# Optimization experiments

Hardware: AMD Instinct MI355X
Metric: run time of the kernel (lower is better)

Reference implementation:

```python
import jax, jax.numpy as jnp
import numpy as np

# CMSBlockLinear block-ELL sparse linear forward.
# values: [R, K, B, B] active weight tiles (out_tile x in_tile)
# col_indices: [R, K] int32, which input block-column each tile multiplies
# y[b,s, r*B+i] = sum_k sum_j values[r,k,i,j] * x[b,s, col_indices[r,k]*B + j] + bias

IN_FEATURES = 2048
OUT_FEATURES = 2048
TILE = 16
DENSITY = 0.25
R = OUT_FEATURES // TILE   # 128
C = IN_FEATURES // TILE    # 128
K = max(1, int(C * DENSITY))  # 32
BATCH, SEQ = 4, 512


def setup_inputs() -> dict:
    key = jax.random.key(0)
    kx, kv, kc = jax.random.split(key, 3)
    x = jax.random.normal(kx, (BATCH, SEQ, IN_FEATURES), dtype=jnp.float32)
    # Kaiming-normal init as in _reset_parameters: std = gain('relu') / sqrt(K*B)
    std = np.sqrt(2.0) / np.sqrt(K * TILE)
    values = jax.random.normal(kv, (R, K, TILE, TILE), dtype=jnp.float32) * std
    # K distinct column indices per row (random topology, as in _initialize_topology)
    rng = np.random.default_rng(0)
    col_np = np.stack([rng.permutation(C)[:K] for _ in range(R)]).astype(np.int32)
    col_indices = jnp.asarray(col_np)
    bias = jnp.zeros((OUT_FEATURES,), dtype=jnp.float32)
    return {"x": x, "values": values, "col_indices": col_indices, "bias": bias}


def reference(x, values, col_indices, bias):
    bs, sl, _ = x.shape
    Rr, Kk, B, _ = values.shape
    Cc = x.shape[-1] // B
    x_blocks = x.reshape(bs, sl, Cc, B)                 # [b, s, C, B]
    # Gather the K active input blocks for every output row: [b, s, R, K, B]
    x_gathered = x_blocks[:, :, col_indices, :]
    # Batched small-block matmul and reduce over K tiles: [b, s, R, B]
    out = jnp.einsum("bsrkj,rkij->bsri", x_gathered, values)
    return out.reshape(bs, sl, Rr * B) + bias
```

## Files before the change

### kernel.cpp

```cpp
#include <hip/hip_runtime.h>
#include <hip/hip_bf16.h>

#define TOKS 2048
#define FEAT 2048
#define NR   128
#define KB   32
#define RB   32
#define TT   32

typedef __attribute__((ext_vector_type(8))) short bf16x8;
typedef __attribute__((ext_vector_type(4))) float f32x4;

__device__ __forceinline__ unsigned short f2bf(float f) {
    unsigned u = __builtin_bit_cast(unsigned, f);
    u += 0x7FFFu + ((u >> 16) & 1u);
    return (unsigned short)(u >> 16);
}

__device__ __forceinline__ bf16x8 pack8(float4 a, float4 b) {
    bf16x8 r;
    r[0] = (short)f2bf(a.x); r[1] = (short)f2bf(a.y);
    r[2] = (short)f2bf(a.z); r[3] = (short)f2bf(a.w);
    r[4] = (short)f2bf(b.x); r[5] = (short)f2bf(b.y);
    r[6] = (short)f2bf(b.z); r[7] = (short)f2bf(b.w);
    return r;
}

__global__ __launch_bounds__(256) void cvt_values_kernel(const float* __restrict__ v,
                                                         unsigned short* __restrict__ o,
                                                         int n) {
    int i = (blockIdx.x * 256 + threadIdx.x) * 4;
    if (i + 3 < n) {
        float4 f = *reinterpret_cast<const float4*>(v + i);
        ushort4 r;
        r.x = f2bf(f.x); r.y = f2bf(f.y); r.z = f2bf(f.z); r.w = f2bf(f.w);
        *reinterpret_cast<ushort4*>(o + i) = r;
    }
}

template<bool VB16>
__global__ __launch_bounds__(512) void bsp_kernel(const float* __restrict__ x,
                                                  const void* __restrict__ values,
                                                  const int* __restrict__ cols,
                                                  const float* __restrict__ bias,
                                                  float* __restrict__ out) {
    __shared__ __align__(16) unsigned short xs[TT * FEAT];

    int bid  = blockIdx.x;
    int xcd  = bid & 7, slot = bid >> 3;
    int tg   = xcd * 8 + (slot >> 2);
    int rg   = slot & 3;
    int tok0 = tg * TT;
    int r0   = rg * RB;
    int tid  = threadIdx.x;

    {
        int tr = tid >> 8;
        int ch = tid & 255;
        #pragma unroll 4
        for (int it = 0; it < TT / 2; ++it) {
            int t = it * 2 + tr;
            const float4* p = reinterpret_cast<const float4*>(
                x + (size_t)(tok0 + t) * FEAT + ch * 8);
            float4 a = p[0], b = p[1];
            int off = (t << 12) + ((ch << 4) ^ ((t & 7) << 4));
            *reinterpret_cast<bf16x8*>(reinterpret_cast<char*>(xs) + off) = pack8(a, b);
        }
    }
    __syncthreads();

    int wave = tid >> 6;
    int lane = tid & 63;
    int n = lane & 15;
    int g = lane >> 4;
    int h = g & 1;
    int q = g >> 1;

    int mrow = n << 12;
    int axor = (n & 7) << 4;

    #pragma unroll 1
    for (int rr = 0; rr < 4; ++rr) {
        int r = r0 + wave * 4 + rr;
        int cbase = __builtin_amdgcn_readfirstlane(r) * KB;

        bf16x8 bfrag[16];
        int aaddr[16];
        if (VB16) {
            const unsigned short* vbl = reinterpret_cast<const unsigned short*>(values)
                + ((size_t)r << 13) + (q << 8) + (n << 4) + (h << 3);
            #pragma unroll
            for (int t = 0; t < 16; ++t) {
                bfrag[t] = *reinterpret_cast<const bf16x8*>(vbl + t * 512);
                int c0 = cols[cbase + 2 * t];
                int c1 = cols[cbase + 2 * t + 1];
                int c  = q ? c1 : c0;
                aaddr[t] = mrow + (((c << 5) + (h << 4)) ^ axor);
            }
        } else {
            const float* vfl = reinterpret_cast<const float*>(values)
                + ((size_t)r << 13) + (q << 8) + (n << 4) + (h << 3);
            #pragma unroll
            for (int t = 0; t < 16; ++t) {
                const float4* pv = reinterpret_cast<const float4*>(vfl + t * 512);
                bfrag[t] = pack8(pv[0], pv[1]);
                int c0 = cols[cbase + 2 * t];
                int c1 = cols[cbase + 2 * t + 1];
                int c  = q ? c1 : c0;
                aaddr[t] = mrow + (((c << 5) + (h << 4)) ^ axor);
            }
        }

        float fb = bias[(r << 4) + n];

        #pragma unroll
        for (int sx = 0; sx < 2; ++sx) {
            f32x4 acc = {0.f, 0.f, 0.f, 0.f};
            const char* xb = reinterpret_cast<const char*>(xs) + (sx << 16);
            #pragma unroll
            for (int t = 0; t < 16; ++t) {
                bf16x8 af = *reinterpret_cast<const bf16x8*>(xb + aaddr[t]);
                acc = __builtin_amdgcn_mfma_f32_16x16x32_bf16(af, bfrag[t], acc, 0, 0, 0);
            }
            int trow = tok0 + (sx << 4) + (g << 2);
            size_t ob = (size_t)trow * 2048 + (r << 4) + n;
            #pragma unroll
            for (int p = 0; p < 4; ++p)
                out[ob + (size_t)p * 2048] = acc[p] + fb;
        }
    }
}

extern "C" void kernel_launch(void* const* d_in, const int* in_sizes, int n_in,
                              void* d_out, int out_size, void* d_ws, size_t ws_size,
                              hipStream_t stream) {
    const float* x      = (const float*)d_in[0];
    const float* values = (const float*)d_in[1];
    const int*   cols   = (const int*)d_in[2];
    const float* bias   = (const float*)d_in[3];
    float*       out    = (float*)d_out;

    const int nv = NR * KB * 16 * 16;
    const int grid = (TOKS / TT) * (NR / RB);

    if (ws_size >= (size_t)nv * sizeof(unsigned short)) {
        unsigned short* vb = (unsigned short*)d_ws;
        cvt_values_kernel<<<nv / (256 * 4), 256, 0, stream>>>(values, vb, nv);
        bsp_kernel<true><<<grid, 512, 0, stream>>>(x, vb, cols, bias, out);
    } else {
        bsp_kernel<false><<<grid, 512, 0, stream>>>(x, values, cols, bias, out);
    }
}
```

Measured before the change: 22.76 us.

## Use 1024-thread blocks, prefetch weight fragments before barrier, split MFMA accumulators

Doubles the block to 16 waves so each wave handles 2 output rows instead of 4, and splits the x staging loop across 4 token rows per iteration. The first row's weight fragments and column addresses are loaded before the LDS barrier, overlapping global loads with the x staging. The MFMA chain is split into two independent accumulators to shorten the dependency chain. The cost is higher register pressure under launch_bounds(1024,4), with a risk of spills.

```diff
diff --git a/kernel.cpp b/kernel.cpp
--- a/kernel.cpp
+++ b/kernel.cpp
@@ -39,11 +39,40 @@
 }
 
 template<bool VB16>
-__global__ __launch_bounds__(512) void bsp_kernel(const float* __restrict__ x,
-                                                  const void* __restrict__ values,
-                                                  const int* __restrict__ cols,
-                                                  const float* __restrict__ bias,
-                                                  float* __restrict__ out) {
+__device__ __forceinline__ void load_frags(const void* __restrict__ values,
+                                           const int* __restrict__ cols,
+                                           int r, int q, int n, int h,
+                                           int mrow, int axor,
+                                           bf16x8* bfrag, int* aaddr) {
+    int cbase = __builtin_amdgcn_readfirstlane(r) * KB;
+    if (VB16) {
+        const unsigned short* vbl = reinterpret_cast<const unsigned short*>(values)
+            + ((size_t)r << 13) + (q << 8) + (n << 4) + (h << 3);
+        #pragma unroll
+        for (int t = 0; t < 16; ++t) {
+            bfrag[t] = *reinterpret_cast<const bf16x8*>(vbl + t * 512);
+            int c = cols[cbase + 2 * t + q];
+            aaddr[t] = mrow + (((c << 5) + (h << 4)) ^ axor);
+        }
+    } else {
+        const float* vfl = reinterpret_cast<const float*>(values)
+            + ((size_t)r << 13) + (q << 8) + (n << 4) + (h << 3);
+        #pragma unroll
+        for (int t = 0; t < 16; ++t) {
+            const float4* pv = reinterpret_cast<const float4*>(vfl + t * 512);
+            bfrag[t] = pack8(pv[0], pv[1]);
+            int c = cols[cbase + 2 * t + q];
+            aaddr[t] = mrow + (((c << 5) + (h << 4)) ^ axor);
+        }
+    }
+}
+
+template<bool VB16>
+__global__ __launch_bounds__(1024, 4) void bsp_kernel(const float* __restrict__ x,
+                                                      const void* __restrict__ values,
+                                                      const int* __restrict__ cols,
+                                                      const float* __restrict__ bias,
+                                                      float* __restrict__ out) {
     __shared__ __align__(16) unsigned short xs[TT * FEAT];
 
     int bid  = blockIdx.x;
@@ -57,9 +86,9 @@
     {
         int tr = tid >> 8;
         int ch = tid & 255;
-        #pragma unroll 4
-        for (int it = 0; it < TT / 2; ++it) {
-            int t = it * 2 + tr;
+        #pragma unroll 2
+        for (int it = 0; it < 8; ++it) {
+            int t = it * 4 + tr;
             const float4* p = reinterpret_cast<const float4*>(
                 x + (size_t)(tok0 + t) * FEAT + ch * 8);
             float4 a = p[0], b = p[1];
@@ -67,7 +96,6 @@
             *reinterpret_cast<bf16x8*>(reinterpret_cast<char*>(xs) + off) = pack8(a, b);
         }
     }
-    __syncthreads();
 
     int wave = tid >> 6;
     int lane = tid & 63;
@@ -79,54 +107,37 @@
     int mrow = n << 12;
     int axor = (n & 7) << 4;
 
+    bf16x8 bfrag[16];
+    int aaddr[16];
+    load_frags<VB16>(values, cols, r0 + wave * 2, q, n, h, mrow, axor, bfrag, aaddr);
+
+    __syncthreads();
+
     #pragma unroll 1
-    for (int rr = 0; rr < 4; ++rr) {
-        int r = r0 + wave * 4 + rr;
-        int cbase = __builtin_amdgcn_readfirstlane(r) * KB;
-
-        bf16x8 bfrag[16];
-        int aaddr[16];
-        if (VB16) {
-            const unsigned short* vbl = reinterpret_cast<const unsigned short*>(values)
-                + ((size_t)r << 13) + (q << 8) + (n << 4) + (h << 3);
-            #pragma unroll
-            for (int t = 0; t < 16; ++t) {
-                bfrag[t] = *reinterpret_cast<const bf16x8*>(vbl + t * 512);
-                int c0 = cols[cbase + 2 * t];
-                int c1 = cols[cbase + 2 * t + 1];
-                int c  = q ? c1 : c0;
-                aaddr[t] = mrow + (((c << 5) + (h << 4)) ^ axor);
-            }
-        } else {
-            const float* vfl = reinterpret_cast<const float*>(values)
-                + ((size_t)r << 13) + (q << 8) + (n << 4) + (h << 3);
-            #pragma unroll
-            for (int t = 0; t < 16; ++t) {
-                const float4* pv = reinterpret_cast<const float4*>(vfl + t * 512);
-                bfrag[t] = pack8(pv[0], pv[1]);
-                int c0 = cols[cbase + 2 * t];
-                int c1 = cols[cbase + 2 * t + 1];
-                int c  = q ? c1 : c0;
-                aaddr[t] = mrow + (((c << 5) + (h << 4)) ^ axor);
-            }
-        }
+    for (int rr = 0; rr < 2; ++rr) {
+        int r = r0 + wave * 2 + rr;
+        if (rr > 0)
+            load_frags<VB16>(values, cols, r, q, n, h, mrow, axor, bfrag, aaddr);
 
         float fb = bias[(r << 4) + n];
 
         #pragma unroll
         for (int sx = 0; sx < 2; ++sx) {
-            f32x4 acc = {0.f, 0.f, 0.f, 0.f};
             const char* xb = reinterpret_cast<const char*>(xs) + (sx << 16);
+            f32x4 acc0 = {0.f, 0.f, 0.f, 0.f};
+            f32x4 acc1 = {0.f, 0.f, 0.f, 0.f};
             #pragma unroll
-            for (int t = 0; t < 16; ++t) {
-                bf16x8 af = *reinterpret_cast<const bf16x8*>(xb + aaddr[t]);
-                acc = __builtin_amdgcn_mfma_f32_16x16x32_bf16(af, bfrag[t], acc, 0, 0, 0);
+            for (int t = 0; t < 8; ++t) {
+                bf16x8 a0 = *reinterpret_cast<const bf16x8*>(xb + aaddr[2 * t]);
+                bf16x8 a1 = *reinterpret_cast<const bf16x8*>(xb + aaddr[2 * t + 1]);
+                acc0 = __builtin_amdgcn_mfma_f32_16x16x32_bf16(a0, bfrag[2 * t],     acc0, 0, 0, 0);
+                acc1 = __builtin_amdgcn_mfma_f32_16x16x32_bf16(a1, bfrag[2 * t + 1], acc1, 0, 0, 0);
             }
             int trow = tok0 + (sx << 4) + (g << 2);
             size_t ob = (size_t)trow * 2048 + (r << 4) + n;
             #pragma unroll
             for (int p = 0; p < 4; ++p)
-                out[ob + (size_t)p * 2048] = acc[p] + fb;
+                out[ob + (size_t)p * 2048] = acc0[p] + acc1[p] + fb;
         }
     }
 }
@@ -146,8 +157,8 @@
     if (ws_size >= (size_t)nv * sizeof(unsigned short)) {
         unsigned short* vb = (unsigned short*)d_ws;
         cvt_values_kernel<<<nv / (256 * 4), 256, 0, stream>>>(values, vb, nv);
-        bsp_kernel<true><<<grid, 512, 0, stream>>>(x, vb, cols, bias, out);
+        bsp_kernel<true><<<grid, 1024, 0, stream>>>(x, vb, cols, bias, out);
     } else {
-        bsp_kernel<false><<<grid, 512, 0, stream>>>(x, values, cols, bias, out);
+        bsp_kernel<false><<<grid, 1024, 0, stream>>>(x, values, cols, bias, out);
     }
 }
```

Result: slower. 24.34 us (+6.9%).

## Drop bf16 values pre-pass, remap blocks per XCD, split MFMA accumulator chain

Applied to the files above, without the earlier changes.

Removes the separate fp32-to-bf16 conversion kernel and its launch, so the main kernel always reads fp32 weights and converts them in registers. Changes the block-to-XCD mapping so each XCD pair handles one row group, letting all blocks on an XCD share the same weight slice in L2. Splits the MFMA reduction into two independent accumulators to shorten the dependency chain. In exchange, every block rereads fp32 weights, which doubles weight traffic compared with bf16.

```diff
diff --git a/kernel.cpp b/kernel.cpp
--- a/kernel.cpp
+++ b/kernel.cpp
@@ -26,30 +26,18 @@
     return r;
 }
 
-__global__ __launch_bounds__(256) void cvt_values_kernel(const float* __restrict__ v,
-                                                         unsigned short* __restrict__ o,
-                                                         int n) {
-    int i = (blockIdx.x * 256 + threadIdx.x) * 4;
-    if (i + 3 < n) {
-        float4 f = *reinterpret_cast<const float4*>(v + i);
-        ushort4 r;
-        r.x = f2bf(f.x); r.y = f2bf(f.y); r.z = f2bf(f.z); r.w = f2bf(f.w);
-        *reinterpret_cast<ushort4*>(o + i) = r;
-    }
-}
-
-template<bool VB16>
-__global__ __launch_bounds__(512) void bsp_kernel(const float* __restrict__ x,
-                                                  const void* __restrict__ values,
-                                                  const int* __restrict__ cols,
-                                                  const float* __restrict__ bias,
-                                                  float* __restrict__ out) {
+__global__ __launch_bounds__(512) void bsp5(const float* __restrict__ x,
+                                            const float* __restrict__ values,
+                                            const int* __restrict__ cols,
+                                            const float* __restrict__ bias,
+                                            float* __restrict__ out) {
     __shared__ __align__(16) unsigned short xs[TT * FEAT];
 
     int bid  = blockIdx.x;
-    int xcd  = bid & 7, slot = bid >> 3;
-    int tg   = xcd * 8 + (slot >> 2);
-    int rg   = slot & 3;
+    int xcd  = bid & 7;
+    int slot = bid >> 3;
+    int rg   = xcd >> 1;
+    int tg   = (xcd & 1) * 32 + slot;
     int tok0 = tg * TT;
     int r0   = rg * RB;
     int tid  = threadIdx.x;
@@ -86,47 +74,36 @@
 
         bf16x8 bfrag[16];
         int aaddr[16];
-        if (VB16) {
-            const unsigned short* vbl = reinterpret_cast<const unsigned short*>(values)
-                + ((size_t)r << 13) + (q << 8) + (n << 4) + (h << 3);
-            #pragma unroll
-            for (int t = 0; t < 16; ++t) {
-                bfrag[t] = *reinterpret_cast<const bf16x8*>(vbl + t * 512);
-                int c0 = cols[cbase + 2 * t];
-                int c1 = cols[cbase + 2 * t + 1];
-                int c  = q ? c1 : c0;
-                aaddr[t] = mrow + (((c << 5) + (h << 4)) ^ axor);
-            }
-        } else {
-            const float* vfl = reinterpret_cast<const float*>(values)
-                + ((size_t)r << 13) + (q << 8) + (n << 4) + (h << 3);
-            #pragma unroll
-            for (int t = 0; t < 16; ++t) {
-                const float4* pv = reinterpret_cast<const float4*>(vfl + t * 512);
-                bfrag[t] = pack8(pv[0], pv[1]);
-                int c0 = cols[cbase + 2 * t];
-                int c1 = cols[cbase + 2 * t + 1];
-                int c  = q ? c1 : c0;
-                aaddr[t] = mrow + (((c << 5) + (h << 4)) ^ axor);
-            }
+        const float* vfl = values + ((size_t)r << 13) + (q << 8) + (n << 4) + (h << 3);
+        #pragma unroll
+        for (int t = 0; t < 16; ++t) {
+            const float4* pv = reinterpret_cast<const float4*>(vfl + t * 512);
+            bfrag[t] = pack8(pv[0], pv[1]);
+            int c0 = cols[cbase + 2 * t];
+            int c1 = cols[cbase + 2 * t + 1];
+            int c  = q ? c1 : c0;
+            aaddr[t] = mrow + (((c << 5) + (h << 4)) ^ axor);
         }
 
         float fb = bias[(r << 4) + n];
 
         #pragma unroll
         for (int sx = 0; sx < 2; ++sx) {
-            f32x4 acc = {0.f, 0.f, 0.f, 0.f};
             const char* xb = reinterpret_cast<const char*>(xs) + (sx << 16);
+            f32x4 acc0 = {0.f, 0.f, 0.f, 0.f};
+            f32x4 acc1 = {0.f, 0.f, 0.f, 0.f};
             #pragma unroll
-            for (int t = 0; t < 16; ++t) {
-                bf16x8 af = *reinterpret_cast<const bf16x8*>(xb + aaddr[t]);
-                acc = __builtin_amdgcn_mfma_f32_16x16x32_bf16(af, bfrag[t], acc, 0, 0, 0);
+            for (int t = 0; t < 8; ++t) {
+                bf16x8 a0 = *reinterpret_cast<const bf16x8*>(xb + aaddr[2 * t]);
+                bf16x8 a1 = *reinterpret_cast<const bf16x8*>(xb + aaddr[2 * t + 1]);
+                acc0 = __builtin_amdgcn_mfma_f32_16x16x32_bf16(a0, bfrag[2 * t],     acc0, 0, 0, 0);
+                acc1 = __builtin_amdgcn_mfma_f32_16x16x32_bf16(a1, bfrag[2 * t + 1], acc1, 0, 0, 0);
             }
             int trow = tok0 + (sx << 4) + (g << 2);
             size_t ob = (size_t)trow * 2048 + (r << 4) + n;
             #pragma unroll
             for (int p = 0; p < 4; ++p)
-                out[ob + (size_t)p * 2048] = acc[p] + fb;
+                out[ob + (size_t)p * 2048] = acc0[p] + acc1[p] + fb;
         }
     }
 }
@@ -140,14 +117,6 @@
     const float* bias   = (const float*)d_in[3];
     float*       out    = (float*)d_out;
 
-    const int nv = NR * KB * 16 * 16;
     const int grid = (TOKS / TT) * (NR / RB);
-
-    if (ws_size >= (size_t)nv * sizeof(unsigned short)) {
-        unsigned short* vb = (unsigned short*)d_ws;
-        cvt_values_kernel<<<nv / (256 * 4), 256, 0, stream>>>(values, vb, nv);
-        bsp_kernel<true><<<grid, 512, 0, stream>>>(x, vb, cols, bias, out);
-    } else {
-        bsp_kernel<false><<<grid, 512, 0, stream>>>(x, values, cols, bias, out);
-    }
+    bsp5<<<grid, 512, 0, stream>>>(x, values, cols, bias, out);
 }
```

Result: slower. 37.55 us (+65.0%).
